# Optimization experiments

Measured on AMD Instinct MI355X. Metric: run time of the kernel, lower is better.

The kernel has to match this reference:

```python
import jax, jax.numpy as jnp
import numpy as np

B, N = 4, 512
D_MODEL, ATOM_CH = 256, 5
PAIR_H, N_RBF, RBF_MAX = 128, 16, 4.0
LN_EPS = 1e-5


def setup_inputs() -> dict:
    key = jax.random.key(0)
    ks = jax.random.split(key, 12)
    sd = 1.0 / np.sqrt(D_MODEL)
    sh = 1.0 / np.sqrt(PAIR_H)
    return {
        "trunk_out": jax.random.normal(ks[0], (B, N, D_MODEL), jnp.float32),
        "coords": jax.random.normal(ks[1], (B, N, 3), jnp.float32),
        "pad_mask": jax.random.randint(ks[2], (B, N), 0, 2).astype(bool),
        "ln_g": jnp.ones((D_MODEL,), jnp.float32),
        "ln_b": jnp.zeros((D_MODEL,), jnp.float32),
        "w_a1": jax.random.normal(ks[3], (D_MODEL, D_MODEL), jnp.float32) * sd,
        "b_a1": jnp.zeros((D_MODEL,), jnp.float32),
        "w_a2": jax.random.normal(ks[4], (D_MODEL, ATOM_CH), jnp.float32) * sd,
        "b_a2": jnp.zeros((ATOM_CH,), jnp.float32),
        "w_pi": jax.random.normal(ks[5], (D_MODEL, PAIR_H), jnp.float32) * sd,
        "w_pj": jax.random.normal(ks[6], (D_MODEL, PAIR_H), jnp.float32) * sd,
        "w_pr": jax.random.normal(ks[7], (N_RBF, PAIR_H), jnp.float32) * 0.25,
        "b_p1": jnp.zeros((PAIR_H,), jnp.float32),
        "w_p2": jax.random.normal(ks[8], (PAIR_H,), jnp.float32) * sh,
        "b_p2": jnp.zeros((1,), jnp.float32),
    }


def _forward(trunk_out, coords, pad_mask, ln_g, ln_b, w_a1, b_a1, w_a2, b_a2,
             w_pi, w_pj, w_pr, b_p1, w_p2, b_p2):
    dt = trunk_out.dtype
    valid = ~pad_mask                                   # (B, N)
    validf = valid.astype(dt)

    # ---- atom head: LayerNorm -> Linear -> SiLU -> Linear, pad-masked ----
    mu = trunk_out.mean(-1, keepdims=True)
    var = jnp.mean((trunk_out - mu) ** 2, -1, keepdims=True)
    xn = (trunk_out - mu) * jax.lax.rsqrt(var + LN_EPS) * ln_g + ln_b
    atom_delta = jax.nn.silu(xn @ w_a1 + b_a1) @ w_a2 + b_a2
    atom_delta = jnp.where(pad_mask[..., None], jnp.zeros((), dt), atom_delta)

    # ---- geometry features (non-periodic adapter) ----
    delta = coords[:, :, None, :] - coords[:, None, :, :]   # (B, N, N, 3)
    sq = jnp.sum(delta * delta, -1)
    dist = jnp.sqrt(jnp.maximum(sq, 1e-12))                 # safe sqrt (diag)
    centers = jnp.linspace(0.0, RBF_MAX, N_RBF, dtype=dt)
    gamma = jnp.asarray(1.0 / (RBF_MAX / max(N_RBF - 1, 1)) ** 2, dt)
    rbf = jnp.exp(-gamma * (dist[..., None] - centers) ** 2)  # (B, N, N, R)
    pair_mask = valid[:, :, None] & valid[:, None, :]

    # ---- pair head: LazyLinear on cat([hi, hj, rbf]) == sum of 3 projections ----
    pi = jnp.einsum('bid,dh->bih', trunk_out, w_pi)         # (B, N, H)
    pj = jnp.einsum('bjd,dh->bjh', trunk_out, w_pj)
    h1 = jax.nn.silu(pi[:, :, None, :] + pj[:, None, :, :]
                     + jnp.einsum('bijr,rh->bijh', rbf, w_pr) + b_p1)
    pw = jnp.einsum('bijh,h->bij', h1, w_p2) + b_p2[0]      # (B, N, N)
    pw = jnp.where(pair_mask, pw, jnp.zeros((), dt))
    pw = jnp.where(jnp.eye(N, dtype=bool), jnp.zeros((), dt), pw)  # zero diag

    # ---- weighted-sum coordinate update ----
    coord_delta = jnp.einsum('bij,bijc->bic', pw, delta)    # (B, N, 3)
    denom = jnp.maximum(validf.sum(1, keepdims=True), 1.0)  # (B, 1)
    coord_delta = coord_delta / denom[..., None]
    coord_delta = jnp.where(pad_mask[..., None], jnp.zeros((), dt), coord_delta)
    mean = (coord_delta * validf[..., None]).sum(1, keepdims=True) / denom[..., None]
    coord_delta = jnp.where(pad_mask[..., None], jnp.zeros((), dt), coord_delta - mean)
    return atom_delta, coord_delta


def reference(trunk_out, coords, pad_mask, ln_g, ln_b, w_a1, b_a1, w_a2, b_a2,
              w_pi, w_pj, w_pr, b_p1, w_p2, b_p2):
    return _forward(trunk_out, coords, pad_mask, ln_g, ln_b, w_a1, b_a1,
                    w_a2, b_a2, w_pi, w_pj, w_pr, b_p1, w_p2, b_p2)
```

## Files before the change

kernel.cpp:

```cpp
#include <hip/hip_runtime.h>
#include <hip/hip_bf16.h>

#define BN 2048
#define NSEQ 512
#define D 256
#define H 128
#define R 16
#define AC 5
#define CHUNK 128
#define ROWG 8
#define SPLIT 4

using bf16 = __hip_bfloat16;

__device__ __forceinline__ float fast_silu(float t) {
    const float e = __expf(-t);
    return t * __builtin_amdgcn_rcpf(1.0f + e);
}
__device__ __forceinline__ float bf2f(unsigned short u) {
    return __uint_as_float(((unsigned)u) << 16);
}

__global__ __launch_bounds__(256) void batch_kernel(
    const int* __restrict__ pad, int* __restrict__ jlist_g, int* __restrict__ M_g)
{
    const int b = blockIdx.x;
    const int tid = threadIdx.x;
    __shared__ int s_wcnt[8];
    __shared__ int s_wbase[8];
    const int wv = tid >> 6, lane = tid & 63;
    unsigned long long bm[2];
    #pragma unroll
    for (int cc = 0; cc < 2; ++cc) {
        const int j = cc * 256 + tid;
        const int ok = (pad[b * NSEQ + j] == 0);
        bm[cc] = __ballot(ok);
        if (lane == 0) s_wcnt[cc * 4 + wv] = __popcll(bm[cc]);
    }
    __syncthreads();
    if (tid == 0) {
        int acc = 0;
        #pragma unroll
        for (int q = 0; q < 8; ++q) { s_wbase[q] = acc; acc += s_wcnt[q]; }
        M_g[b] = acc;
    }
    __syncthreads();
    #pragma unroll
    for (int cc = 0; cc < 2; ++cc) {
        const int j = cc * 256 + tid;
        if (pad[b * NSEQ + j] == 0) {
            const int pos = s_wbase[cc * 4 + wv]
                          + __popcll(bm[cc] & ((1ull << lane) - 1ull));
            jlist_g[b * NSEQ + pos] = j;
        }
    }
}

__global__ __launch_bounds__(512) void row_kernel(
    const float* __restrict__ trunk, const int* __restrict__ pad,
    const float* __restrict__ ln_g, const float* __restrict__ ln_b,
    const float* __restrict__ w_a1, const float* __restrict__ b_a1,
    const float* __restrict__ w_a2, const float* __restrict__ b_a2,
    const float* __restrict__ w_pi, const float* __restrict__ w_pj,
    const float* __restrict__ b_p1,
    float* __restrict__ out_atom, float* __restrict__ pj_o,
    unsigned short* __restrict__ pib_o)
{
    const int row0 = blockIdx.x * ROWG;
    const int tid = threadIdx.x;
    const int wv = tid >> 6, lane = tid & 63;
    __shared__ __align__(16) float x_t[2][D][4];
    __shared__ __align__(16) float xn_t[2][D][4];
    __shared__ float y[ROWG][D];
    __shared__ float mu_s[ROWG], rs_s[ROWG];

    #pragma unroll
    for (int gg = 0; gg < 4; ++gg) {
        const int g = gg * 2 + (tid >> 8);
        const int e = tid & 255;
        x_t[g >> 2][e][g & 3] = trunk[(size_t)(row0 + g) * D + e];
    }
    __syncthreads();

    {
        const int g = wv;
        float s = 0.0f, ss = 0.0f;
        #pragma unroll
        for (int e2 = lane; e2 < D; e2 += 64) {
            const float v = x_t[g >> 2][e2][g & 3];
            s += v; ss += v * v;
        }
        #pragma unroll
        for (int off = 32; off; off >>= 1) {
            s  += __shfl_xor(s, off);
            ss += __shfl_xor(ss, off);
        }
        if (lane == 0) {
            const float mu  = s * (1.0f / D);
            const float var = ss * (1.0f / D) - mu * mu;
            mu_s[g] = mu;
            rs_s[g] = rsqrtf(var + 1e-5f);
        }
    }
    __syncthreads();
    #pragma unroll
    for (int gg = 0; gg < 4; ++gg) {
        const int g = gg * 2 + (tid >> 8);
        const int e = tid & 255;
        xn_t[g >> 2][e][g & 3] =
            (x_t[g >> 2][e][g & 3] - mu_s[g]) * rs_s[g] * ln_g[e] + ln_b[e];
    }
    __syncthreads();

    if (tid < 256) {
        const float bb = b_a1[tid];
        float a0 = bb, a1v = bb, a2v = bb, a3 = bb, a4 = bb, a5 = bb, a6 = bb, a7 = bb;
        for (int d = 0; d < D; ++d) {
            const float w = w_a1[d * D + tid];
            const float4 lo = *(const float4*)xn_t[0][d];
            const float4 hi = *(const float4*)xn_t[1][d];
            a0  = fmaf(lo.x, w, a0);  a1v = fmaf(lo.y, w, a1v);
            a2v = fmaf(lo.z, w, a2v); a3  = fmaf(lo.w, w, a3);
            a4  = fmaf(hi.x, w, a4);  a5  = fmaf(hi.y, w, a5);
            a6  = fmaf(hi.z, w, a6);  a7  = fmaf(hi.w, w, a7);
        }
        y[0][tid] = a0  / (1.0f + expf(-a0));
        y[1][tid] = a1v / (1.0f + expf(-a1v));
        y[2][tid] = a2v / (1.0f + expf(-a2v));
        y[3][tid] = a3  / (1.0f + expf(-a3));
        y[4][tid] = a4  / (1.0f + expf(-a4));
        y[5][tid] = a5  / (1.0f + expf(-a5));
        y[6][tid] = a6  / (1.0f + expf(-a6));
        y[7][tid] = a7  / (1.0f + expf(-a7));
    } else if (tid < 384) {
        const int h = tid - 256;
        float p0 = 0.f, p1 = 0.f, p2 = 0.f, p3 = 0.f, p4 = 0.f, p5 = 0.f, p6 = 0.f, p7 = 0.f;
        for (int d = 0; d < D; ++d) {
            const float w = w_pi[d * H + h];
            const float4 lo = *(const float4*)x_t[0][d];
            const float4 hi = *(const float4*)x_t[1][d];
            p0 = fmaf(lo.x, w, p0); p1 = fmaf(lo.y, w, p1);
            p2 = fmaf(lo.z, w, p2); p3 = fmaf(lo.w, w, p3);
            p4 = fmaf(hi.x, w, p4); p5 = fmaf(hi.y, w, p5);
            p6 = fmaf(hi.z, w, p6); p7 = fmaf(hi.w, w, p7);
        }
        const float bb = b_p1[h];
        const float pv[ROWG] = {p0 + bb, p1 + bb, p2 + bb, p3 + bb,
                                p4 + bb, p5 + bb, p6 + bb, p7 + bb};
        #pragma unroll
        for (int g = 0; g < ROWG; ++g) {
            const bf16 pb = __float2bfloat16(pv[g]);
            pib_o[(size_t)(row0 + g) * H + h] = *(const unsigned short*)&pb;
        }
    } else {
        const int h = tid - 384;
        float p0 = 0.f, p1 = 0.f, p2 = 0.f, p3 = 0.f, p4 = 0.f, p5 = 0.f, p6 = 0.f, p7 = 0.f;
        for (int d = 0; d < D; ++d) {
            const float w = w_pj[d * H + h];
            const float4 lo = *(const float4*)x_t[0][d];
            const float4 hi = *(const float4*)x_t[1][d];
            p0 = fmaf(lo.x, w, p0); p1 = fmaf(lo.y, w, p1);
            p2 = fmaf(lo.z, w, p2); p3 = fmaf(lo.w, w, p3);
            p4 = fmaf(hi.x, w, p4); p5 = fmaf(hi.y, w, p5);
            p6 = fmaf(hi.z, w, p6); p7 = fmaf(hi.w, w, p7);
        }
        const float pv[ROWG] = {p0, p1, p2, p3, p4, p5, p6, p7};
        #pragma unroll
        for (int g = 0; g < ROWG; ++g)
            pj_o[(size_t)(row0 + g) * H + h] = pv[g];
    }
    __syncthreads();

    if (tid < ROWG * AC) {
        const int g = tid / AC, c = tid % AC;
        float a = b_a2[c];
        for (int d = 0; d < D; ++d) a = fmaf(y[g][d], w_a2[d * AC + c], a);
        out_atom[(row0 + g) * AC + c] = (pad[row0 + g] != 0) ? 0.0f : a;
    }
}

__device__ __forceinline__ void pair_body(
    const float pvx, const float pvy,
    const float* __restrict__ rbf_row, const float4 dk,
    const float pibx, const float piby,
    const float* wprA, const float* wprB, const float2 wp22,
    float& cdx, float& cdy, float& cdz,
    float& sdx, float& sdy, float& sdz)
{
    float t0a = pibx + pvx, t0b = 0.0f;
    float t1a = piby + pvy, t1b = 0.0f;
    #pragma unroll
    for (int r = 0; r < R; r += 2) {
        const float qa = rbf_row[r];
        const float qb = rbf_row[r + 1];
        t0a = fmaf(qa, wprA[r],     t0a);
        t0b = fmaf(qb, wprA[r + 1], t0b);
        t1a = fmaf(qa, wprB[r],     t1a);
        t1b = fmaf(qb, wprB[r + 1], t1b);
    }
    const float u0 = fast_silu(t0a + t0b);
    const float u1 = fast_silu(t1a + t1b);
    const float part = u0 * wp22.x + u1 * wp22.y;
    cdx = fmaf(part, dk.x, cdx);
    cdy = fmaf(part, dk.y, cdy);
    cdz = fmaf(part, dk.z, cdz);
    sdx += dk.x; sdy += dk.y; sdz += dk.z;
}

__global__ __launch_bounds__(256) void pair_kernel(
    const float* __restrict__ coords, const int* __restrict__ pad,
    const float* __restrict__ w_pr, const float* __restrict__ w_p2,
    const float* __restrict__ b_p2,
    const float* __restrict__ pj_i, const unsigned short* __restrict__ pib_i,
    const int* __restrict__ jlist_g, const int* __restrict__ M_g,
    float* __restrict__ cd_part)
{
    const int row  = blockIdx.x >> 2;
    const int part_id = blockIdx.x & 3;
    const int b = row >> 9;
    const int tid = threadIdx.x;

    if (pad[row] != 0) {
        if (tid == 0) {
            cd_part[(row * SPLIT + part_id) * 3 + 0] = 0.0f;
            cd_part[(row * SPLIT + part_id) * 3 + 1] = 0.0f;
            cd_part[(row * SPLIT + part_id) * 3 + 2] = 0.0f;
        }
        return;
    }

    __shared__ __align__(16) float s_rbf[CHUNK][20];
    __shared__ __align__(16) float4 s_d4[CHUNK];
    __shared__ int   s_jl[CHUNK];
    __shared__ float rw1[4], rw2[4], rw3[4];

    const int wv = tid >> 6, lane = tid & 63;
    const int M = M_g[b];
    const int Mq  = (M + SPLIT - 1) / SPLIT;
    const int kLo = part_id * Mq;
    const int kHi = min(M, kLo + Mq);

    float wprA[R], wprB[R];
    #pragma unroll
    for (int r = 0; r < R; ++r) {
        const float2 wv2 = ((const float2*)(w_pr + r * H))[lane];
        wprA[r] = wv2.x;
        wprB[r] = wv2.y;
    }
    const ushort2 pibu = ((const ushort2*)(pib_i + (size_t)row * H))[lane];
    const float pibx = bf2f(pibu.x), piby = bf2f(pibu.y);
    const float2 wp22 = ((const float2*)w_p2)[lane];
    const float bp2 = b_p2[0];
    const float cix = coords[(size_t)row * 3 + 0];
    const float ciy = coords[(size_t)row * 3 + 1];
    const float ciz = coords[(size_t)row * 3 + 2];

    float cdx = 0.0f, cdy = 0.0f, cdz = 0.0f;
    float sdx = 0.0f, sdy = 0.0f, sdz = 0.0f;
    const float* pjb = pj_i + (size_t)b * NSEQ * H;
    const float gamma = 14.0625f;

    for (int c0 = kLo; c0 < kHi; c0 += CHUNK) {
        const int cn = (kHi - c0 < CHUNK) ? (kHi - c0) : CHUNK;
        __syncthreads();
        if (tid < cn) {
            const int j = jlist_g[b * NSEQ + c0 + tid];
            s_jl[tid] = j;
            const float* cj = coords + (size_t)(b * NSEQ + j) * 3;
            const float dx = cix - cj[0];
            const float dy = ciy - cj[1];
            const float dz = ciz - cj[2];
            const float sq = dx * dx + dy * dy + dz * dz;
            const float dist = sqrtf(fmaxf(sq, 1e-12f));
            s_d4[tid] = make_float4(dx, dy, dz, 0.0f);
            #pragma unroll
            for (int c = 0; c < 4; ++c) {
                float4 q;
                const float t0 = dist - (float)(4.0 * (4 * c + 0) / 15.0);
                const float t1 = dist - (float)(4.0 * (4 * c + 1) / 15.0);
                const float t2 = dist - (float)(4.0 * (4 * c + 2) / 15.0);
                const float t3 = dist - (float)(4.0 * (4 * c + 3) / 15.0);
                q.x = __expf(-gamma * t0 * t0);
                q.y = __expf(-gamma * t1 * t1);
                q.z = __expf(-gamma * t2 * t2);
                q.w = __expf(-gamma * t3 * t3);
                *(float4*)(&s_rbf[tid][4 * c]) = q;
            }
        }
        __syncthreads();

        const int cl = cn - 1;
        int k = wv;
        float2 pv0 = ((const float2*)(pjb + (size_t)s_jl[min(k,      cl)] * H))[lane];
        float2 pv1 = ((const float2*)(pjb + (size_t)s_jl[min(k + 4,  cl)] * H))[lane];
        float2 pv2 = ((const float2*)(pjb + (size_t)s_jl[min(k + 8,  cl)] * H))[lane];
        float2 pv3 = ((const float2*)(pjb + (size_t)s_jl[min(k + 12, cl)] * H))[lane];
        for (; k < cn; k += 16) {
            const int kn = k + 16;
            const float2 nv0 = ((const float2*)(pjb + (size_t)s_jl[min(kn,      cl)] * H))[lane];
            const float2 nv1 = ((const float2*)(pjb + (size_t)s_jl[min(kn + 4,  cl)] * H))[lane];
            const float2 nv2 = ((const float2*)(pjb + (size_t)s_jl[min(kn + 8,  cl)] * H))[lane];
            const float2 nv3 = ((const float2*)(pjb + (size_t)s_jl[min(kn + 12, cl)] * H))[lane];

            const int k1 = k + 4, k2 = k + 8, k3 = k + 12;
            pair_body(pv0.x, pv0.y, s_rbf[k], s_d4[k], pibx, piby,
                      wprA, wprB, wp22, cdx, cdy, cdz, sdx, sdy, sdz);
            if (k1 < cn) pair_body(pv1.x, pv1.y, s_rbf[k1], s_d4[k1], pibx, piby,
                                   wprA, wprB, wp22, cdx, cdy, cdz, sdx, sdy, sdz);
            if (k2 < cn) pair_body(pv2.x, pv2.y, s_rbf[k2], s_d4[k2], pibx, piby,
                                   wprA, wprB, wp22, cdx, cdy, cdz, sdx, sdy, sdz);
            if (k3 < cn) pair_body(pv3.x, pv3.y, s_rbf[k3], s_d4[k3], pibx, piby,
                                   wprA, wprB, wp22, cdx, cdy, cdz, sdx, sdy, sdz);
            pv0 = nv0; pv1 = nv1; pv2 = nv2; pv3 = nv3;
        }
    }
    #pragma unroll
    for (int off = 32; off; off >>= 1) {
        cdx += __shfl_xor(cdx, off);
        cdy += __shfl_xor(cdy, off);
        cdz += __shfl_xor(cdz, off);
    }
    if (lane == 0) {
        rw1[wv] = cdx + bp2 * sdx;
        rw2[wv] = cdy + bp2 * sdy;
        rw3[wv] = cdz + bp2 * sdz;
    }
    __syncthreads();
    if (tid == 0) {
        cd_part[(row * SPLIT + part_id) * 3 + 0] = rw1[0] + rw1[1] + rw1[2] + rw1[3];
        cd_part[(row * SPLIT + part_id) * 3 + 1] = rw2[0] + rw2[1] + rw2[2] + rw2[3];
        cd_part[(row * SPLIT + part_id) * 3 + 2] = rw3[0] + rw3[1] + rw3[2] + rw3[3];
    }
}

__global__ __launch_bounds__(256) void finalize_kernel(
    const float* __restrict__ cd_part, const int* __restrict__ pad,
    float* __restrict__ out_coord)
{
    const int b = blockIdx.x;
    const int tid = threadIdx.x;
    __shared__ float r1[256], r2[256], r3[256], r4[256];
    float sx = 0.0f, sy = 0.0f, sz = 0.0f, cnt = 0.0f;
    for (int ii = tid; ii < NSEQ; ii += 256) {
        const int row = b * NSEQ + ii;
        if (pad[row] == 0) {
            float cx = 0.0f, cy = 0.0f, cz = 0.0f;
            #pragma unroll
            for (int q = 0; q < SPLIT; ++q) {
                cx += cd_part[(row * SPLIT + q) * 3 + 0];
                cy += cd_part[(row * SPLIT + q) * 3 + 1];
                cz += cd_part[(row * SPLIT + q) * 3 + 2];
            }
            sx += cx; sy += cy; sz += cz;
            cnt += 1.0f;
        }
    }
    r1[tid] = sx; r2[tid] = sy; r3[tid] = sz; r4[tid] = cnt;
    __syncthreads();
    for (int s = 128; s > 0; s >>= 1) {
        if (tid < s) {
            r1[tid] += r1[tid + s]; r2[tid] += r2[tid + s];
            r3[tid] += r3[tid + s]; r4[tid] += r4[tid + s];
        }
        __syncthreads();
    }
    const float denom = fmaxf(r4[0], 1.0f);
    const float inv_d = 1.0f / denom;
    const float mx = r1[0] * inv_d * inv_d;
    const float my = r2[0] * inv_d * inv_d;
    const float mz = r3[0] * inv_d * inv_d;
    for (int ii = tid; ii < NSEQ; ii += 256) {
        const int row = b * NSEQ + ii;
        const bool v = (pad[row] == 0);
        float cx = 0.0f, cy = 0.0f, cz = 0.0f;
        #pragma unroll
        for (int q = 0; q < SPLIT; ++q) {
            cx += cd_part[(row * SPLIT + q) * 3 + 0];
            cy += cd_part[(row * SPLIT + q) * 3 + 1];
            cz += cd_part[(row * SPLIT + q) * 3 + 2];
        }
        out_coord[row * 3 + 0] = v ? cx * inv_d - mx : 0.0f;
        out_coord[row * 3 + 1] = v ? cy * inv_d - my : 0.0f;
        out_coord[row * 3 + 2] = v ? cz * inv_d - mz : 0.0f;
    }
}

extern "C" void kernel_launch(void* const* d_in, const int* in_sizes, int n_in,
                              void* d_out, int out_size, void* d_ws, size_t ws_size,
                              hipStream_t stream) {
    const float* trunk  = (const float*)d_in[0];
    const float* coords = (const float*)d_in[1];
    const int*   pad    = (const int*)d_in[2];
    const float* ln_g   = (const float*)d_in[3];
    const float* ln_b   = (const float*)d_in[4];
    const float* w_a1   = (const float*)d_in[5];
    const float* b_a1   = (const float*)d_in[6];
    const float* w_a2   = (const float*)d_in[7];
    const float* b_a2   = (const float*)d_in[8];
    const float* w_pi   = (const float*)d_in[9];
    const float* w_pj   = (const float*)d_in[10];
    const float* w_pr   = (const float*)d_in[11];
    const float* b_p1   = (const float*)d_in[12];
    const float* w_p2   = (const float*)d_in[13];
    const float* b_p2   = (const float*)d_in[14];

    float* out_atom  = (float*)d_out;
    float* out_coord = out_atom + (size_t)BN * AC;

    int*   jlist_g = (int*)d_ws;
    int*   M_g     = jlist_g + 4 * NSEQ;
    float* cd_part = (float*)(M_g + 16);
    float* pj_buf  = cd_part + (size_t)BN * SPLIT * 3;
    unsigned short* pib_buf = (unsigned short*)(pj_buf + (size_t)BN * H);

    batch_kernel<<<4, 256, 0, stream>>>(pad, jlist_g, M_g);
    row_kernel<<<BN / ROWG, 512, 0, stream>>>(trunk, pad, ln_g, ln_b, w_a1, b_a1,
                                              w_a2, b_a2, w_pi, w_pj, b_p1,
                                              out_atom, pj_buf, pib_buf);
    pair_kernel<<<BN * SPLIT, 256, 0, stream>>>(coords, pad, w_pr, w_p2, b_p2,
                                                pj_buf, pib_buf, jlist_g, M_g, cd_part);
    finalize_kernel<<<4, 256, 0, stream>>>(cd_part, pad, out_coord);
}
```

Measured before the change: 68.25 us.

## Hoist b_p2 delta-sum term out of pair loop and store pj in bf16

```diff
diff --git a/kernel.cpp b/kernel.cpp
--- a/kernel.cpp
+++ b/kernel.cpp
@@ -20,29 +20,49 @@
 __device__ __forceinline__ float bf2f(unsigned short u) {
     return __uint_as_float(((unsigned)u) << 16);
 }
+__device__ __forceinline__ unsigned short f2bu(float v) {
+    const bf16 pb = __float2bfloat16(v);
+    return *(const unsigned short*)&pb;
+}
 
 __global__ __launch_bounds__(256) void batch_kernel(
-    const int* __restrict__ pad, int* __restrict__ jlist_g, int* __restrict__ M_g)
+    const int* __restrict__ pad, const float* __restrict__ coords,
+    int* __restrict__ jlist_g, int* __restrict__ M_g, float* __restrict__ csum_g)
 {
     const int b = blockIdx.x;
     const int tid = threadIdx.x;
     __shared__ int s_wcnt[8];
     __shared__ int s_wbase[8];
+    __shared__ float r1[256], r2[256], r3[256];
     const int wv = tid >> 6, lane = tid & 63;
     unsigned long long bm[2];
+    float sx = 0.0f, sy = 0.0f, sz = 0.0f;
     #pragma unroll
     for (int cc = 0; cc < 2; ++cc) {
         const int j = cc * 256 + tid;
         const int ok = (pad[b * NSEQ + j] == 0);
         bm[cc] = __ballot(ok);
         if (lane == 0) s_wcnt[cc * 4 + wv] = __popcll(bm[cc]);
-    }
-    __syncthreads();
+        if (ok) {
+            sx += coords[(size_t)(b * NSEQ + j) * 3 + 0];
+            sy += coords[(size_t)(b * NSEQ + j) * 3 + 1];
+            sz += coords[(size_t)(b * NSEQ + j) * 3 + 2];
+        }
+    }
+    r1[tid] = sx; r2[tid] = sy; r3[tid] = sz;
+    __syncthreads();
+    for (int s = 128; s > 0; s >>= 1) {
+        if (tid < s) { r1[tid] += r1[tid + s]; r2[tid] += r2[tid + s]; r3[tid] += r3[tid + s]; }
+        __syncthreads();
+    }
     if (tid == 0) {
         int acc = 0;
         #pragma unroll
         for (int q = 0; q < 8; ++q) { s_wbase[q] = acc; acc += s_wcnt[q]; }
         M_g[b] = acc;
+        csum_g[b * 3 + 0] = r1[0];
+        csum_g[b * 3 + 1] = r2[0];
+        csum_g[b * 3 + 2] = r3[0];
     }
     __syncthreads();
     #pragma unroll
@@ -63,7 +83,7 @@
     const float* __restrict__ w_a2, const float* __restrict__ b_a2,
     const float* __restrict__ w_pi, const float* __restrict__ w_pj,
     const float* __restrict__ b_p1,
-    float* __restrict__ out_atom, float* __restrict__ pj_o,
+    float* __restrict__ out_atom, unsigned short* __restrict__ pj_o,
     unsigned short* __restrict__ pib_o)
 {
     const int row0 = blockIdx.x * ROWG;
@@ -148,10 +168,8 @@
         const float pv[ROWG] = {p0 + bb, p1 + bb, p2 + bb, p3 + bb,
                                 p4 + bb, p5 + bb, p6 + bb, p7 + bb};
         #pragma unroll
-        for (int g = 0; g < ROWG; ++g) {
-            const bf16 pb = __float2bfloat16(pv[g]);
-            pib_o[(size_t)(row0 + g) * H + h] = *(const unsigned short*)&pb;
-        }
+        for (int g = 0; g < ROWG; ++g)
+            pib_o[(size_t)(row0 + g) * H + h] = f2bu(pv[g]);
     } else {
         const int h = tid - 384;
         float p0 = 0.f, p1 = 0.f, p2 = 0.f, p3 = 0.f, p4 = 0.f, p5 = 0.f, p6 = 0.f, p7 = 0.f;
@@ -167,7 +185,7 @@
         const float pv[ROWG] = {p0, p1, p2, p3, p4, p5, p6, p7};
         #pragma unroll
         for (int g = 0; g < ROWG; ++g)
-            pj_o[(size_t)(row0 + g) * H + h] = pv[g];
+            pj_o[(size_t)(row0 + g) * H + h] = f2bu(pv[g]);
     }
     __syncthreads();
 
@@ -184,8 +202,7 @@
     const float* __restrict__ rbf_row, const float4 dk,
     const float pibx, const float piby,
     const float* wprA, const float* wprB, const float2 wp22,
-    float& cdx, float& cdy, float& cdz,
-    float& sdx, float& sdy, float& sdz)
+    float& cdx, float& cdy, float& cdz)
 {
     float t0a = pibx + pvx, t0b = 0.0f;
     float t1a = piby + pvy, t1b = 0.0f;
@@ -204,14 +221,12 @@
     cdx = fmaf(part, dk.x, cdx);
     cdy = fmaf(part, dk.y, cdy);
     cdz = fmaf(part, dk.z, cdz);
-    sdx += dk.x; sdy += dk.y; sdz += dk.z;
 }
 
 __global__ __launch_bounds__(256) void pair_kernel(
     const float* __restrict__ coords, const int* __restrict__ pad,
     const float* __restrict__ w_pr, const float* __restrict__ w_p2,
-    const float* __restrict__ b_p2,
-    const float* __restrict__ pj_i, const unsigned short* __restrict__ pib_i,
+    const unsigned short* __restrict__ pj_i, const unsigned short* __restrict__ pib_i,
     const int* __restrict__ jlist_g, const int* __restrict__ M_g,
     float* __restrict__ cd_part)
 {
@@ -250,14 +265,12 @@
     const ushort2 pibu = ((const ushort2*)(pib_i + (size_t)row * H))[lane];
     const float pibx = bf2f(pibu.x), piby = bf2f(pibu.y);
     const float2 wp22 = ((const float2*)w_p2)[lane];
-    const float bp2 = b_p2[0];
     const float cix = coords[(size_t)row * 3 + 0];
     const float ciy = coords[(size_t)row * 3 + 1];
     const float ciz = coords[(size_t)row * 3 + 2];
 
     float cdx = 0.0f, cdy = 0.0f, cdz = 0.0f;
-    float sdx = 0.0f, sdy = 0.0f, sdz = 0.0f;
-    const float* pjb = pj_i + (size_t)b * NSEQ * H;
+    const unsigned short* pjb = pj_i + (size_t)b * NSEQ * H;
     const float gamma = 14.0625f;
 
     for (int c0 = kLo; c0 < kHi; c0 += CHUNK) {
@@ -291,26 +304,26 @@
 
         const int cl = cn - 1;
         int k = wv;
-        float2 pv0 = ((const float2*)(pjb + (size_t)s_jl[min(k,      cl)] * H))[lane];
-        float2 pv1 = ((const float2*)(pjb + (size_t)s_jl[min(k + 4,  cl)] * H))[lane];
-        float2 pv2 = ((const float2*)(pjb + (size_t)s_jl[min(k + 8,  cl)] * H))[lane];
-        float2 pv3 = ((const float2*)(pjb + (size_t)s_jl[min(k + 12, cl)] * H))[lane];
+        ushort2 pv0 = ((const ushort2*)(pjb + (size_t)s_jl[min(k,      cl)] * H))[lane];
+        ushort2 pv1 = ((const ushort2*)(pjb + (size_t)s_jl[min(k + 4,  cl)] * H))[lane];
+        ushort2 pv2 = ((const ushort2*)(pjb + (size_t)s_jl[min(k + 8,  cl)] * H))[lane];
+        ushort2 pv3 = ((const ushort2*)(pjb + (size_t)s_jl[min(k + 12, cl)] * H))[lane];
         for (; k < cn; k += 16) {
             const int kn = k + 16;
-            const float2 nv0 = ((const float2*)(pjb + (size_t)s_jl[min(kn,      cl)] * H))[lane];
-            const float2 nv1 = ((const float2*)(pjb + (size_t)s_jl[min(kn + 4,  cl)] * H))[lane];
-            const float2 nv2 = ((const float2*)(pjb + (size_t)s_jl[min(kn + 8,  cl)] * H))[lane];
-            const float2 nv3 = ((const float2*)(pjb + (size_t)s_jl[min(kn + 12, cl)] * H))[lane];
+            const ushort2 nv0 = ((const ushort2*)(pjb + (size_t)s_jl[min(kn,      cl)] * H))[lane];
+            const ushort2 nv1 = ((const ushort2*)(pjb + (size_t)s_jl[min(kn + 4,  cl)] * H))[lane];
+            const ushort2 nv2 = ((const ushort2*)(pjb + (size_t)s_jl[min(kn + 8,  cl)] * H))[lane];
+            const ushort2 nv3 = ((const ushort2*)(pjb + (size_t)s_jl[min(kn + 12, cl)] * H))[lane];
 
             const int k1 = k + 4, k2 = k + 8, k3 = k + 12;
-            pair_body(pv0.x, pv0.y, s_rbf[k], s_d4[k], pibx, piby,
-                      wprA, wprB, wp22, cdx, cdy, cdz, sdx, sdy, sdz);
-            if (k1 < cn) pair_body(pv1.x, pv1.y, s_rbf[k1], s_d4[k1], pibx, piby,
-                                   wprA, wprB, wp22, cdx, cdy, cdz, sdx, sdy, sdz);
-            if (k2 < cn) pair_body(pv2.x, pv2.y, s_rbf[k2], s_d4[k2], pibx, piby,
-                                   wprA, wprB, wp22, cdx, cdy, cdz, sdx, sdy, sdz);
-            if (k3 < cn) pair_body(pv3.x, pv3.y, s_rbf[k3], s_d4[k3], pibx, piby,
-                                   wprA, wprB, wp22, cdx, cdy, cdz, sdx, sdy, sdz);
+            pair_body(bf2f(pv0.x), bf2f(pv0.y), s_rbf[k], s_d4[k], pibx, piby,
+                      wprA, wprB, wp22, cdx, cdy, cdz);
+            if (k1 < cn) pair_body(bf2f(pv1.x), bf2f(pv1.y), s_rbf[k1], s_d4[k1], pibx, piby,
+                                   wprA, wprB, wp22, cdx, cdy, cdz);
+            if (k2 < cn) pair_body(bf2f(pv2.x), bf2f(pv2.y), s_rbf[k2], s_d4[k2], pibx, piby,
+                                   wprA, wprB, wp22, cdx, cdy, cdz);
+            if (k3 < cn) pair_body(bf2f(pv3.x), bf2f(pv3.y), s_rbf[k3], s_d4[k3], pibx, piby,
+                                   wprA, wprB, wp22, cdx, cdy, cdz);
             pv0 = nv0; pv1 = nv1; pv2 = nv2; pv3 = nv3;
         }
     }
@@ -320,11 +333,7 @@
         cdy += __shfl_xor(cdy, off);
         cdz += __shfl_xor(cdz, off);
     }
-    if (lane == 0) {
-        rw1[wv] = cdx + bp2 * sdx;
-        rw2[wv] = cdy + bp2 * sdy;
-        rw3[wv] = cdz + bp2 * sdz;
-    }
+    if (lane == 0) { rw1[wv] = cdx; rw2[wv] = cdy; rw3[wv] = cdz; }
     __syncthreads();
     if (tid == 0) {
         cd_part[(row * SPLIT + part_id) * 3 + 0] = rw1[0] + rw1[1] + rw1[2] + rw1[3];
@@ -335,16 +344,26 @@
 
 __global__ __launch_bounds__(256) void finalize_kernel(
     const float* __restrict__ cd_part, const int* __restrict__ pad,
+    const float* __restrict__ coords, const int* __restrict__ M_g,
+    const float* __restrict__ csum_g, const float* __restrict__ b_p2,
     float* __restrict__ out_coord)
 {
     const int b = blockIdx.x;
     const int tid = threadIdx.x;
-    __shared__ float r1[256], r2[256], r3[256], r4[256];
-    float sx = 0.0f, sy = 0.0f, sz = 0.0f, cnt = 0.0f;
+    __shared__ float r1[256], r2[256], r3[256];
+    const float bp2 = b_p2[0];
+    const float Mf  = (float)M_g[b];
+    const float csx = csum_g[b * 3 + 0];
+    const float csy = csum_g[b * 3 + 1];
+    const float csz = csum_g[b * 3 + 2];
+
+    float sx = 0.0f, sy = 0.0f, sz = 0.0f;
     for (int ii = tid; ii < NSEQ; ii += 256) {
         const int row = b * NSEQ + ii;
         if (pad[row] == 0) {
-            float cx = 0.0f, cy = 0.0f, cz = 0.0f;
+            float cx = bp2 * fmaf(Mf, coords[(size_t)row * 3 + 0], -csx);
+            float cy = bp2 * fmaf(Mf, coords[(size_t)row * 3 + 1], -csy);
+            float cz = bp2 * fmaf(Mf, coords[(size_t)row * 3 + 2], -csz);
             #pragma unroll
             for (int q = 0; q < SPLIT; ++q) {
                 cx += cd_part[(row * SPLIT + q) * 3 + 0];
@@ -352,36 +371,39 @@
                 cz += cd_part[(row * SPLIT + q) * 3 + 2];
             }
             sx += cx; sy += cy; sz += cz;
-            cnt += 1.0f;
-        }
-    }
-    r1[tid] = sx; r2[tid] = sy; r3[tid] = sz; r4[tid] = cnt;
+        }
+    }
+    r1[tid] = sx; r2[tid] = sy; r3[tid] = sz;
     __syncthreads();
     for (int s = 128; s > 0; s >>= 1) {
-        if (tid < s) {
-            r1[tid] += r1[tid + s]; r2[tid] += r2[tid + s];
-            r3[tid] += r3[tid + s]; r4[tid] += r4[tid + s];
-        }
+        if (tid < s) { r1[tid] += r1[tid + s]; r2[tid] += r2[tid + s]; r3[tid] += r3[tid + s]; }
         __syncthreads();
     }
-    const float denom = fmaxf(r4[0], 1.0f);
+    const float denom = fmaxf(Mf, 1.0f);
     const float inv_d = 1.0f / denom;
     const float mx = r1[0] * inv_d * inv_d;
     const float my = r2[0] * inv_d * inv_d;
     const float mz = r3[0] * inv_d * inv_d;
     for (int ii = tid; ii < NSEQ; ii += 256) {
         const int row = b * NSEQ + ii;
-        const bool v = (pad[row] == 0);
-        float cx = 0.0f, cy = 0.0f, cz = 0.0f;
-        #pragma unroll
-        for (int q = 0; q < SPLIT; ++q) {
-            cx += cd_part[(row * SPLIT + q) * 3 + 0];
-            cy += cd_part[(row * SPLIT + q) * 3 + 1];
-            cz += cd_part[(row * SPLIT + q) * 3 + 2];
-        }
-        out_coord[row * 3 + 0] = v ? cx * inv_d - mx : 0.0f;
-        out_coord[row * 3 + 1] = v ? cy * inv_d - my : 0.0f;
-        out_coord[row * 3 + 2] = v ? cz * inv_d - mz : 0.0f;
+        if (pad[row] == 0) {
+            float cx = bp2 * fmaf(Mf, coords[(size_t)row * 3 + 0], -csx);
+            float cy = bp2 * fmaf(Mf, coords[(size_t)row * 3 + 1], -csy);
+            float cz = bp2 * fmaf(Mf, coords[(size_t)row * 3 + 2], -csz);
+            #pragma unroll
+            for (int q = 0; q < SPLIT; ++q) {
+                cx += cd_part[(row * SPLIT + q) * 3 + 0];
+                cy += cd_part[(row * SPLIT + q) * 3 + 1];
+                cz += cd_part[(row * SPLIT + q) * 3 + 2];
+            }
+            out_coord[row * 3 + 0] = cx * inv_d - mx;
+            out_coord[row * 3 + 1] = cy * inv_d - my;
+            out_coord[row * 3 + 2] = cz * inv_d - mz;
+        } else {
+            out_coord[row * 3 + 0] = 0.0f;
+            out_coord[row * 3 + 1] = 0.0f;
+            out_coord[row * 3 + 2] = 0.0f;
+        }
     }
 }
 
@@ -409,15 +431,17 @@
 
     int*   jlist_g = (int*)d_ws;
     int*   M_g     = jlist_g + 4 * NSEQ;
-    float* cd_part = (float*)(M_g + 16);
-    float* pj_buf  = cd_part + (size_t)BN * SPLIT * 3;
-    unsigned short* pib_buf = (unsigned short*)(pj_buf + (size_t)BN * H);
-
-    batch_kernel<<<4, 256, 0, stream>>>(pad, jlist_g, M_g);
+    float* csum_g  = (float*)(M_g + 16);
+    float* cd_part = csum_g + 16;
+    unsigned short* pj_buf  = (unsigned short*)(cd_part + (size_t)BN * SPLIT * 3);
+    unsigned short* pib_buf = pj_buf + (size_t)BN * H;
+
+    batch_kernel<<<4, 256, 0, stream>>>(pad, coords, jlist_g, M_g, csum_g);
     row_kernel<<<BN / ROWG, 512, 0, stream>>>(trunk, pad, ln_g, ln_b, w_a1, b_a1,
                                               w_a2, b_a2, w_pi, w_pj, b_p1,
                                               out_atom, pj_buf, pib_buf);
-    pair_kernel<<<BN * SPLIT, 256, 0, stream>>>(coords, pad, w_pr, w_p2, b_p2,
+    pair_kernel<<<BN * SPLIT, 256, 0, stream>>>(coords, pad, w_pr, w_p2,
                                                 pj_buf, pib_buf, jlist_g, M_g, cd_part);
-    finalize_kernel<<<4, 256, 0, stream>>>(cd_part, pad, out_coord);
-}
+    finalize_kernel<<<4, 256, 0, stream>>>(cd_part, pad, coords, M_g, csum_g,
+                                           b_p2, out_coord);
+}
```

Result: faster. 66.43 us, median of 2 (-2.7%).
